# Optimization experiments

Hardware: AMD Instinct MI355X
Metric: run time of the kernel (lower is better)

## Reference

```python
import jax, jax.numpy as jnp
import numpy as np

B, H, E, L = 2048, 4096, 8, 512
TAU = 1.0


def setup_inputs() -> dict:
    key = jax.random.key(0)
    k1, k2, k3, k4 = jax.random.split(key, 4)
    hidden = jax.random.normal(k1, (B, H), dtype=jnp.float32)
    envs = jax.random.normal(k2, (B, E), dtype=jnp.float32)
    idx = jnp.arange(B, dtype=jnp.int64)
    gumbel = jax.random.gumbel(k3, (B, E), dtype=jnp.float32)
    W = jax.random.normal(k4, (E, L, H), dtype=jnp.float32) * (1.0 / np.sqrt(H))
    return {"hidden": hidden, "envs": envs, "idx": idx, "gumbel": gumbel, "W": W}


def _hard_gumbel_softmax(log_probs, gumbel, tau):
    # F.gumbel_softmax(log_probs, tau=1, hard=True) with pre-sampled gumbel noise
    y_soft = jax.nn.softmax((log_probs + gumbel) / tau, axis=-1)
    y_hard = jax.nn.one_hot(jnp.argmax(y_soft, axis=-1), y_soft.shape[-1], dtype=y_soft.dtype)
    # straight-through estimator
    return y_hard + y_soft - jax.lax.stop_gradient(y_soft)


def reference(hidden, envs, idx, gumbel, W):
    # gating: env = gumbel_softmax(log_softmax(envs[idx]))  -> [B, E]
    log_probs = jax.nn.log_softmax(envs[idx], axis=-1)
    env = _hard_gumbel_softmax(log_probs, gumbel, TAU)
    # per-expert logits: [B, E, L]; fuses the per-sample python loop
    expert_logits = jnp.einsum("bh,elh->bel", hidden, W)
    # gating combine: [B, L]
    logits = jnp.einsum("be,bel->bl", env, expert_logits)
    # variance penalty over expert weights
    W_mean = jnp.mean(W, axis=0)  # [L, H]
    diff_sq = jnp.sum((W - W_mean[None]) ** 2, axis=(1, 2))  # ||W_e - W_mean||_2^2 per expert
    l1 = jnp.sum(jnp.abs(W), axis=(1, 2))                    # ||W_e||_1 per expert
    loss_penalty = jnp.mean(diff_sq / (l1 ** 2))
    return logits, loss_penalty
```

## Files before the change

### kernel.cpp

```cpp
#include <hip/hip_runtime.h>
#include <hip/hip_bf16.h>

constexpr int B = 2048, H = 4096, E = 8, L = 512;
constexpr int LH = L * H;

typedef float f4v __attribute__((ext_vector_type(4)));
typedef short short8 __attribute__((ext_vector_type(8)));

constexpr int BT = 128;
constexpr int LT = 128;
constexpr int KT = 32;
constexpr int SK = 4;
constexpr int RTMAX = 3;
constexpr int NITER = (H / SK) / KT;

constexpr int NGEMM = 4 * 2 * 4 * 4 * RTMAX;

constexpr int Q = LH / 4;
constexpr int QSHARE = (Q + NGEMM - 1) / NGEMM;
constexpr int NSTRIP = (QSHARE + 255) / 256;

constexpr size_t WS_COUNTS = 0;
constexpr size_t WS_ACCUM = 32;
constexpr size_t WS_ROWLIST = 96;
constexpr size_t WS_ZERO_BYTES = 96;

using as1_u32 = const __attribute__((address_space(1))) unsigned int;
using as3_u32 = __attribute__((address_space(3))) unsigned int;

static __device__ __forceinline__ void dma16(const float* g, float* lds) {
  __builtin_amdgcn_global_load_lds((as1_u32*)g, (as3_u32*)lds, 16, 0, 0);
}

static __device__ __forceinline__ unsigned pk2(float a, float b) {
  __hip_bfloat162 p = __float22bfloat162_rn(make_float2(a, b));
  unsigned u;
  __builtin_memcpy(&u, &p, 4);
  return u;
}

static __device__ __forceinline__ short8 cvt8(f4v lo, f4v hi) {
  union { short8 s; unsigned u[4]; } r;
  r.u[0] = pk2(lo.x, lo.y);
  r.u[1] = pk2(lo.z, lo.w);
  r.u[2] = pk2(hi.x, hi.y);
  r.u[3] = pk2(hi.z, hi.w);
  return r.s;
}

__global__ void gating_kernel(const float* __restrict__ envs,
                              const float* __restrict__ gumbel,
                              int* __restrict__ counts,
                              int* __restrict__ row_list) {
  int b = blockIdx.x * blockDim.x + threadIdx.x;
  if (b >= B) return;
  float zmax = -1e30f;
  int am = 0;
#pragma unroll
  for (int e = 0; e < E; ++e) {
    float z = envs[b * E + e] + gumbel[b * E + e];
    if (z > zmax) { zmax = z; am = e; }
  }
  int pos = atomicAdd(&counts[am], 1);
  row_list[am * B + pos] = b;
}

__launch_bounds__(256, 2)
__global__ void fused_kernel(const float* __restrict__ hidden,
                             const float* __restrict__ W,
                             const int* __restrict__ counts,
                             const int* __restrict__ row_list,
                             float* __restrict__ out,
                             float* __restrict__ accum) {
  const int id = blockIdx.x;
  const int t = threadIdx.x;

  __shared__ __align__(16) float AshF[2][BT * KT];
  __shared__ __align__(16) float BshF[2][LT * KT];
  __shared__ int rlsh[BT];
  __shared__ float red[4][16];

  const int q0 = id * QSHARE;
  const int share = (Q - q0 < QSHARE) ? (Q - q0) : QSHARE;
  float dacc[E], lacc[E];
#pragma unroll
  for (int e = 0; e < E; ++e) { dacc[e] = 0.f; lacc[e] = 0.f; }

  float4 pw[E];
  float pv = 0.f;

  auto pen_issue = [&](int s) {
    int off = s * 256 + t;
    pv = (off < share) ? 1.f : 0.f;
    int p = q0 + ((off < share) ? off : 0);
#pragma unroll
    for (int e = 0; e < E; ++e)
      pw[e] = *(const float4*)(W + (size_t)e * LH + (size_t)p * 4);
  };
  auto pen_consume = [&]() {
    float mx = 0.f, my = 0.f, mz = 0.f, mw = 0.f;
#pragma unroll
    for (int e = 0; e < E; ++e) {
      mx += pw[e].x; my += pw[e].y; mz += pw[e].z; mw += pw[e].w;
    }
    mx *= 0.125f; my *= 0.125f; mz *= 0.125f; mw *= 0.125f;
#pragma unroll
    for (int e = 0; e < E; ++e) {
      float dx = pw[e].x - mx, dy = pw[e].y - my, dz = pw[e].z - mz,
            dw = pw[e].w - mw;
      dacc[e] += pv * (dx * dx + dy * dy + dz * dz + dw * dw);
      lacc[e] += pv * (fabsf(pw[e].x) + fabsf(pw[e].y) + fabsf(pw[e].z) +
                       fabsf(pw[e].w));
    }
  };
  auto pen_reduce = [&]() {
    float vals[16];
#pragma unroll
    for (int e = 0; e < E; ++e) { vals[e] = dacc[e]; vals[8 + e] = lacc[e]; }
#pragma unroll
    for (int k = 0; k < 16; ++k) {
      float v = vals[k];
      for (int off = 32; off > 0; off >>= 1) v += __shfl_xor(v, off);
      vals[k] = v;
    }
    const int wv = t >> 6, lane = t & 63;
    if (lane == 0) {
#pragma unroll
      for (int k = 0; k < 16; ++k) red[wv][k] = vals[k];
    }
    __syncthreads();
    if (t < 16) {
      atomicAdd(&accum[t], red[0][t] + red[1][t] + red[2][t] + red[3][t]);
    }
  };

  const int lt = id & 3;
  const int ep = (id >> 2) & 1;
  const int sk = (id >> 3) & 3;
  const int eh = (id >> 5) & 3;
  const int rt = id >> 7;
  const int e = eh * 2 + ep;

  const int cnt = counts[e];
  const int rbase = rt * BT;

  if (rbase >= cnt) {
#pragma unroll
    for (int s = 0; s < NSTRIP; ++s) {
      pen_issue(s);
      pen_consume();
    }
    pen_reduce();
    return;
  }
  const int lbase = lt * LT;

  if (t < BT) {
    int rr = rbase + t;
    rlsh[t] = row_list[e * B + (rr < cnt ? rr : (cnt - 1))];
  }
  __syncthreads();

  const float* Wp = W + (size_t)e * LH + (size_t)lbase * H;

  const int wave = t >> 6;
  const int lane = t & 63;
  const int quad = lane >> 4;
  const int l16 = lane & 15;
  const int wm = (wave >> 1) * 64;
  const int wn = (wave & 1) * 64;

  const int kbeg = sk * (H / SK);
  const int srow = lane >> 3;
  const int sblk = lane & 7;

  const float* sp[8];
  float* sl[2][8];
  const bool stageA = (wave < 2);
#pragma unroll
  for (int i = 0; i < 8; ++i) {
    int r = (stageA ? wave : (wave - 2)) * 64 + i * 8 + srow;
    int gblk = sblk ^ (r & 7);
    if (stageA) {
      sp[i] = hidden + (size_t)rlsh[r] * H + kbeg + gblk * 4;
      sl[0][i] = &AshF[0][(r - srow) * KT];
      sl[1][i] = &AshF[1][(r - srow) * KT];
    } else {
      sp[i] = Wp + (size_t)r * H + kbeg + gblk * 4;
      sl[0][i] = &BshF[0][(r - srow) * KT];
      sl[1][i] = &BshF[1][(r - srow) * KT];
    }
  }

  auto stage = [&](int buf) {
#pragma unroll
    for (int i = 0; i < 8; ++i) {
      dma16(sp[i], sl[buf][i]);
      sp[i] += KT;
    }
  };

  const int r7 = l16 & 7;
  const int slo = (2 * quad) ^ r7;
  const int shi = slo ^ 1;

  f4v acc[4][4] = {};

  stage(0);

  for (int it = 0; it < NITER; ++it) {
    const int buf = it & 1;
    __syncthreads();
    if (it + 1 < NITER) stage(buf ^ 1);

    if (!(it & 1) && (it >> 1) < NSTRIP) pen_issue(it >> 1);

    short8 af[4], bf[4];
#pragma unroll
    for (int i = 0; i < 4; ++i) {
      int ra = wm + i * 16 + l16;
      f4v lo = *(const f4v*)&AshF[buf][ra * KT + slo * 4];
      f4v hi = *(const f4v*)&AshF[buf][ra * KT + shi * 4];
      af[i] = cvt8(lo, hi);
    }
#pragma unroll
    for (int j = 0; j < 4; ++j) {
      int rb = wn + j * 16 + l16;
      f4v lo = *(const f4v*)&BshF[buf][rb * KT + slo * 4];
      f4v hi = *(const f4v*)&BshF[buf][rb * KT + shi * 4];
      bf[j] = cvt8(lo, hi);
    }

    if ((it & 1) && (it >> 1) < NSTRIP) pen_consume();

#pragma unroll
    for (int i = 0; i < 4; ++i)
#pragma unroll
      for (int j = 0; j < 4; ++j)
        acc[i][j] =
            __builtin_amdgcn_mfma_f32_16x16x32_bf16(af[i], bf[j], acc[i][j],
                                                    0, 0, 0);
  }

#pragma unroll
  for (int i = 0; i < 4; ++i) {
#pragma unroll
    for (int j = 0; j < 4; ++j) {
#pragma unroll
      for (int reg = 0; reg < 4; ++reg) {
        int rloc = wm + i * 16 + quad * 4 + reg;
        if (rbase + rloc < cnt) {
          int bidx = rlsh[rloc];
          atomicAdd(&out[(size_t)bidx * L + lbase + wn + j * 16 + l16],
                    acc[i][j][reg]);
        }
      }
    }
  }

  __syncthreads();
  pen_reduce();
}

__global__ void finalize_kernel(const float* __restrict__ accum,
                                float* __restrict__ out) {
  if (threadIdx.x == 0) {
    float loss = 0.f;
#pragma unroll
    for (int e = 0; e < E; ++e) {
      float l1 = accum[8 + e];
      loss += accum[e] / (l1 * l1);
    }
    out[(size_t)B * L] = loss * 0.125f;
  }
}

extern "C" void kernel_launch(void* const* d_in, const int* in_sizes, int n_in,
                              void* d_out, int out_size, void* d_ws, size_t ws_size,
                              hipStream_t stream) {
  (void)in_sizes; (void)n_in; (void)ws_size;
  const float* hidden = (const float*)d_in[0];
  const float* envs   = (const float*)d_in[1];
  const float* gumbel = (const float*)d_in[3];
  const float* W      = (const float*)d_in[4];
  float* out = (float*)d_out;

  char* ws = (char*)d_ws;
  int*   counts   = (int*)(ws + WS_COUNTS);
  float* accum    = (float*)(ws + WS_ACCUM);
  int*   row_list = (int*)(ws + WS_ROWLIST);

  (void)hipMemsetAsync(d_ws, 0, WS_ZERO_BYTES, stream);
  (void)hipMemsetAsync(d_out, 0, (size_t)out_size * sizeof(float), stream);

  gating_kernel<<<dim3(B / 256), dim3(256), 0, stream>>>(envs, gumbel, counts,
                                                         row_list);

  fused_kernel<<<dim3(NGEMM), dim3(256), 0, stream>>>(hidden, W, counts,
                                                      row_list, out, accum);

  finalize_kernel<<<dim3(1), dim3(64), 0, stream>>>(accum, out);
}
```

Baseline: 187.8 us.

## Pre-convert W and hidden to bf16 in a prep pass, then run a bf16 GEMM

Adds a prep kernel that computes the variance/L1 penalty and writes bf16 copies of W and hidden into workspace. A new GEMM kernel reads the bf16 data with a larger K tile and triple-buffered async LDS staging, with explicit vmcnt waits. This removes the per-iteration fp32-to-bf16 conversion and halves the bytes the GEMM streams. In exchange it adds an extra full read and write pass over W and hidden, and it needs a large workspace; the old fused kernel is kept as a fallback when the workspace is too small.

```diff
diff --git a/kernel.cpp b/kernel.cpp
--- a/kernel.cpp
+++ b/kernel.cpp
@@ -6,29 +6,19 @@
 
 typedef float f4v __attribute__((ext_vector_type(4)));
 typedef short short8 __attribute__((ext_vector_type(8)));
-
-constexpr int BT = 128;
-constexpr int LT = 128;
-constexpr int KT = 32;
-constexpr int SK = 4;
-constexpr int RTMAX = 3;
-constexpr int NITER = (H / SK) / KT;
-
-constexpr int NGEMM = 4 * 2 * 4 * 4 * RTMAX;
-
-constexpr int Q = LH / 4;
-constexpr int QSHARE = (Q + NGEMM - 1) / NGEMM;
-constexpr int NSTRIP = (QSHARE + 255) / 256;
 
 constexpr size_t WS_COUNTS = 0;
 constexpr size_t WS_ACCUM = 32;
 constexpr size_t WS_ROWLIST = 96;
 constexpr size_t WS_ZERO_BYTES = 96;
+constexpr size_t WS_WBF = 65792;
+constexpr size_t WS_HBF = WS_WBF + (size_t)LH * E * 2;
+constexpr size_t WS_TOTAL_NEW = WS_HBF + (size_t)B * H * 2;
 
 using as1_u32 = const __attribute__((address_space(1))) unsigned int;
 using as3_u32 = __attribute__((address_space(3))) unsigned int;
 
-static __device__ __forceinline__ void dma16(const float* g, float* lds) {
+static __device__ __forceinline__ void dma16(const void* g, void* lds) {
   __builtin_amdgcn_global_load_lds((as1_u32*)g, (as3_u32*)lds, 16, 0, 0);
 }
 
@@ -64,6 +54,199 @@
   int pos = atomicAdd(&counts[am], 1);
   row_list[am * B + pos] = b;
 }
+
+__launch_bounds__(256)
+__global__ void prep_kernel(const float* __restrict__ W,
+                            const float* __restrict__ hidden,
+                            unsigned short* __restrict__ Wbf,
+                            unsigned short* __restrict__ hbf,
+                            float* __restrict__ accum) {
+  const int t = threadIdx.x;
+  const int p = blockIdx.x * 256 + t;
+
+  float4 w[E];
+  float mx = 0.f, my = 0.f, mz = 0.f, mw = 0.f;
+#pragma unroll
+  for (int e = 0; e < E; ++e) {
+    w[e] = *(const float4*)(W + (size_t)e * LH + (size_t)p * 4);
+    mx += w[e].x; my += w[e].y; mz += w[e].z; mw += w[e].w;
+  }
+  mx *= 0.125f; my *= 0.125f; mz *= 0.125f; mw *= 0.125f;
+
+  float vals[16];
+#pragma unroll
+  for (int e = 0; e < E; ++e) {
+    float dx = w[e].x - mx, dy = w[e].y - my, dz = w[e].z - mz,
+          dw = w[e].w - mw;
+    vals[e] = dx * dx + dy * dy + dz * dz + dw * dw;
+    vals[8 + e] = fabsf(w[e].x) + fabsf(w[e].y) + fabsf(w[e].z) + fabsf(w[e].w);
+    uint2 pk = {pk2(w[e].x, w[e].y), pk2(w[e].z, w[e].w)};
+    *(uint2*)(Wbf + (size_t)e * LH + (size_t)p * 4) = pk;
+  }
+
+#pragma unroll
+  for (int j = 0; j < 4; ++j) {
+    size_t q = (size_t)blockIdx.x * 1024 + j * 256 + t;
+    float4 hv = *(const float4*)(hidden + q * 4);
+    uint2 pk = {pk2(hv.x, hv.y), pk2(hv.z, hv.w)};
+    *(uint2*)(hbf + q * 4) = pk;
+  }
+
+#pragma unroll
+  for (int k = 0; k < 16; ++k) {
+    float v = vals[k];
+    for (int off = 32; off > 0; off >>= 1) v += __shfl_xor(v, off);
+    vals[k] = v;
+  }
+  __shared__ float red[4][16];
+  const int wv = t >> 6, lane = t & 63;
+  if (lane == 0) {
+#pragma unroll
+    for (int k = 0; k < 16; ++k) red[wv][k] = vals[k];
+  }
+  __syncthreads();
+  if (t < 16)
+    atomicAdd(&accum[t], red[0][t] + red[1][t] + red[2][t] + red[3][t]);
+}
+
+constexpr int BT = 128, LT = 128, KTB = 64;
+constexpr int SK = 4;
+constexpr int RTMAX = 3;
+constexpr int NITER = (H / SK) / KTB;
+constexpr int NGEMM = 4 * 2 * 4 * 4 * RTMAX;
+
+__launch_bounds__(256, 1)
+__global__ void gemm_bf_kernel(const unsigned short* __restrict__ hbf,
+                               const unsigned short* __restrict__ Wbf,
+                               const int* __restrict__ counts,
+                               const int* __restrict__ row_list,
+                               float* __restrict__ out) {
+  const int id = blockIdx.x;
+  const int t = threadIdx.x;
+
+  __shared__ __align__(16) unsigned short Ash[3][BT * KTB];
+  __shared__ __align__(16) unsigned short Bsh[3][LT * KTB];
+  __shared__ int rlsh[BT];
+
+  const int lt = id & 3;
+  const int ep = (id >> 2) & 1;
+  const int sk = (id >> 3) & 3;
+  const int eh = (id >> 5) & 3;
+  const int rt = id >> 7;
+  const int e = eh * 2 + ep;
+
+  const int cnt = counts[e];
+  const int rbase = rt * BT;
+  if (rbase >= cnt) return;
+  const int lbase = lt * LT;
+
+  if (t < BT) {
+    int rr = rbase + t;
+    rlsh[t] = row_list[e * B + (rr < cnt ? rr : (cnt - 1))];
+  }
+  __syncthreads();
+
+  const unsigned short* Wp = Wbf + (size_t)e * LH + (size_t)lbase * H;
+
+  const int wave = t >> 6;
+  const int lane = t & 63;
+  const int quad = lane >> 4;
+  const int l16 = lane & 15;
+  const int wm = (wave >> 1) * 64;
+  const int wn = (wave & 1) * 64;
+
+  const int kbeg = sk * (H / SK);
+  const int srow = lane >> 3;
+  const int sblk = lane & 7;
+
+  const unsigned short* sp[8];
+  unsigned short* sl[3][8];
+  const bool stageA = (wave < 2);
+#pragma unroll
+  for (int i = 0; i < 8; ++i) {
+    int r = (stageA ? wave : (wave - 2)) * 64 + i * 8 + srow;
+    int gblk = sblk ^ (r & 7);
+    if (stageA) {
+      sp[i] = hbf + (size_t)rlsh[r] * H + kbeg + gblk * 8;
+      sl[0][i] = &Ash[0][(r - srow) * KTB];
+      sl[1][i] = &Ash[1][(r - srow) * KTB];
+      sl[2][i] = &Ash[2][(r - srow) * KTB];
+    } else {
+      sp[i] = Wp + (size_t)r * H + kbeg + gblk * 8;
+      sl[0][i] = &Bsh[0][(r - srow) * KTB];
+      sl[1][i] = &Bsh[1][(r - srow) * KTB];
+      sl[2][i] = &Bsh[2][(r - srow) * KTB];
+    }
+  }
+
+  auto stage = [&](int buf) {
+#pragma unroll
+    for (int i = 0; i < 8; ++i) {
+      dma16(sp[i], sl[buf][i]);
+      sp[i] += KTB;
+    }
+  };
+
+  const int r7 = l16 & 7;
+  f4v acc[4][4] = {};
+
+  stage(0);
+  stage(1);
+
+#pragma unroll
+  for (int it = 0; it < NITER; ++it) {
+    const int buf = it % 3;
+    if (it < NITER - 1) {
+      __asm__ __volatile__("s_waitcnt vmcnt(8)\n\ts_barrier" ::: "memory");
+    } else {
+      __asm__ __volatile__("s_waitcnt vmcnt(0)\n\ts_barrier" ::: "memory");
+    }
+    if (it + 2 < NITER) stage((it + 2) % 3);
+
+#pragma unroll
+    for (int kk = 0; kk < 2; ++kk) {
+      short8 af[4], bfr[4];
+#pragma unroll
+      for (int i = 0; i < 4; ++i) {
+        int slot = (kk * 4 + quad) ^ r7;
+        af[i] = *(const short8*)&Ash[buf][(wm + i * 16 + l16) * KTB + slot * 8];
+      }
+#pragma unroll
+      for (int j = 0; j < 4; ++j) {
+        int slot = (kk * 4 + quad) ^ r7;
+        bfr[j] = *(const short8*)&Bsh[buf][(wn + j * 16 + l16) * KTB + slot * 8];
+      }
+#pragma unroll
+      for (int i = 0; i < 4; ++i)
+#pragma unroll
+        for (int j = 0; j < 4; ++j)
+          acc[i][j] = __builtin_amdgcn_mfma_f32_16x16x32_bf16(
+              af[i], bfr[j], acc[i][j], 0, 0, 0);
+    }
+  }
+
+#pragma unroll
+  for (int i = 0; i < 4; ++i) {
+#pragma unroll
+    for (int j = 0; j < 4; ++j) {
+#pragma unroll
+      for (int reg = 0; reg < 4; ++reg) {
+        int rloc = wm + i * 16 + quad * 4 + reg;
+        if (rbase + rloc < cnt) {
+          int bidx = rlsh[rloc];
+          atomicAdd(&out[(size_t)bidx * L + lbase + wn + j * 16 + l16],
+                    acc[i][j][reg]);
+        }
+      }
+    }
+  }
+}
+
+constexpr int KTF = 32;
+constexpr int NITERF = (H / SK) / KTF;
+constexpr int Q = LH / 4;
+constexpr int QSHARE = (Q + NGEMM - 1) / NGEMM;
+constexpr int NSTRIP = (QSHARE + 255) / 256;
 
 __launch_bounds__(256, 2)
 __global__ void fused_kernel(const float* __restrict__ hidden,
@@ -75,8 +258,8 @@
   const int id = blockIdx.x;
   const int t = threadIdx.x;
 
-  __shared__ __align__(16) float AshF[2][BT * KT];
-  __shared__ __align__(16) float BshF[2][LT * KT];
+  __shared__ __align__(16) float AshF[2][BT * KTF];
+  __shared__ __align__(16) float BshF[2][LT * KTF];
   __shared__ int rlsh[BT];
   __shared__ float red[4][16];
 
@@ -85,7 +268,6 @@
   float dacc[E], lacc[E];
 #pragma unroll
   for (int e = 0; e < E; ++e) { dacc[e] = 0.f; lacc[e] = 0.f; }
-
   float4 pw[E];
   float pv = 0.f;
 
@@ -129,9 +311,8 @@
       for (int k = 0; k < 16; ++k) red[wv][k] = vals[k];
     }
     __syncthreads();
-    if (t < 16) {
+    if (t < 16)
       atomicAdd(&accum[t], red[0][t] + red[1][t] + red[2][t] + red[3][t]);
-    }
   };
 
   const int lt = id & 3;
@@ -146,10 +327,7 @@
 
   if (rbase >= cnt) {
 #pragma unroll
-    for (int s = 0; s < NSTRIP; ++s) {
-      pen_issue(s);
-      pen_consume();
-    }
+    for (int s = 0; s < NSTRIP; ++s) { pen_issue(s); pen_consume(); }
     pen_reduce();
     return;
   }
@@ -162,7 +340,6 @@
   __syncthreads();
 
   const float* Wp = W + (size_t)e * LH + (size_t)lbase * H;
-
   const int wave = t >> 6;
   const int lane = t & 63;
   const int quad = lane >> 4;
@@ -183,12 +360,12 @@
     int gblk = sblk ^ (r & 7);
     if (stageA) {
       sp[i] = hidden + (size_t)rlsh[r] * H + kbeg + gblk * 4;
-      sl[0][i] = &AshF[0][(r - srow) * KT];
-      sl[1][i] = &AshF[1][(r - srow) * KT];
+      sl[0][i] = &AshF[0][(r - srow) * KTF];
+      sl[1][i] = &AshF[1][(r - srow) * KTF];
     } else {
       sp[i] = Wp + (size_t)r * H + kbeg + gblk * 4;
-      sl[0][i] = &BshF[0][(r - srow) * KT];
-      sl[1][i] = &BshF[1][(r - srow) * KT];
+      sl[0][i] = &BshF[0][(r - srow) * KTF];
+      sl[1][i] = &BshF[1][(r - srow) * KTF];
     }
   }
 
@@ -196,7 +373,7 @@
 #pragma unroll
     for (int i = 0; i < 8; ++i) {
       dma16(sp[i], sl[buf][i]);
-      sp[i] += KT;
+      sp[i] += KTF;
     }
   };
 
@@ -205,41 +382,37 @@
   const int shi = slo ^ 1;
 
   f4v acc[4][4] = {};
-
   stage(0);
 
-  for (int it = 0; it < NITER; ++it) {
+  for (int it = 0; it < NITERF; ++it) {
     const int buf = it & 1;
     __syncthreads();
-    if (it + 1 < NITER) stage(buf ^ 1);
-
+    if (it + 1 < NITERF) stage(buf ^ 1);
     if (!(it & 1) && (it >> 1) < NSTRIP) pen_issue(it >> 1);
 
     short8 af[4], bf[4];
 #pragma unroll
     for (int i = 0; i < 4; ++i) {
       int ra = wm + i * 16 + l16;
-      f4v lo = *(const f4v*)&AshF[buf][ra * KT + slo * 4];
-      f4v hi = *(const f4v*)&AshF[buf][ra * KT + shi * 4];
+      f4v lo = *(const f4v*)&AshF[buf][ra * KTF + slo * 4];
+      f4v hi = *(const f4v*)&AshF[buf][ra * KTF + shi * 4];
       af[i] = cvt8(lo, hi);
     }
 #pragma unroll
     for (int j = 0; j < 4; ++j) {
       int rb = wn + j * 16 + l16;
-      f4v lo = *(const f4v*)&BshF[buf][rb * KT + slo * 4];
-      f4v hi = *(const f4v*)&BshF[buf][rb * KT + shi * 4];
+      f4v lo = *(const f4v*)&BshF[buf][rb * KTF + slo * 4];
+      f4v hi = *(const f4v*)&BshF[buf][rb * KTF + shi * 4];
       bf[j] = cvt8(lo, hi);
     }
-
     if ((it & 1) && (it >> 1) < NSTRIP) pen_consume();
 
 #pragma unroll
     for (int i = 0; i < 4; ++i)
 #pragma unroll
       for (int j = 0; j < 4; ++j)
-        acc[i][j] =
-            __builtin_amdgcn_mfma_f32_16x16x32_bf16(af[i], bf[j], acc[i][j],
-                                                    0, 0, 0);
+        acc[i][j] = __builtin_amdgcn_mfma_f32_16x16x32_bf16(af[i], bf[j],
+                                                            acc[i][j], 0, 0, 0);
   }
 
 #pragma unroll
@@ -257,7 +430,6 @@
       }
     }
   }
-
   __syncthreads();
   pen_reduce();
 }
@@ -278,7 +450,7 @@
 extern "C" void kernel_launch(void* const* d_in, const int* in_sizes, int n_in,
                               void* d_out, int out_size, void* d_ws, size_t ws_size,
                               hipStream_t stream) {
-  (void)in_sizes; (void)n_in; (void)ws_size;
+  (void)in_sizes; (void)n_in;
   const float* hidden = (const float*)d_in[0];
   const float* envs   = (const float*)d_in[1];
   const float* gumbel = (const float*)d_in[3];
@@ -289,6 +461,8 @@
   int*   counts   = (int*)(ws + WS_COUNTS);
   float* accum    = (float*)(ws + WS_ACCUM);
   int*   row_list = (int*)(ws + WS_ROWLIST);
+  unsigned short* Wbf = (unsigned short*)(ws + WS_WBF);
+  unsigned short* hbf = (unsigned short*)(ws + WS_HBF);
 
   (void)hipMemsetAsync(d_ws, 0, WS_ZERO_BYTES, stream);
   (void)hipMemsetAsync(d_out, 0, (size_t)out_size * sizeof(float), stream);
@@ -296,8 +470,15 @@
   gating_kernel<<<dim3(B / 256), dim3(256), 0, stream>>>(envs, gumbel, counts,
                                                          row_list);
 
-  fused_kernel<<<dim3(NGEMM), dim3(256), 0, stream>>>(hidden, W, counts,
-                                                      row_list, out, accum);
+  if (ws_size >= WS_TOTAL_NEW) {
+    prep_kernel<<<dim3(2048), dim3(256), 0, stream>>>(W, hidden, Wbf, hbf,
+                                                      accum);
+    gemm_bf_kernel<<<dim3(NGEMM), dim3(256), 0, stream>>>(hbf, Wbf, counts,
+                                                          row_list, out);
+  } else {
+    fused_kernel<<<dim3(NGEMM), dim3(256), 0, stream>>>(hidden, W, counts,
+                                                        row_list, out, accum);
+  }
 
   finalize_kernel<<<dim3(1), dim3(64), 0, stream>>>(accum, out);
 }
```

Result: slower. 198.0 us (+5.4%).
